# Optimization experiments

Hardware: AMD Instinct MI355X
Metric: run time of the kernel (lower is better)

The kernel has to match this reference:

```python
import jax, jax.numpy as jnp
import numpy as np


def setup_inputs() -> dict:
    key = jax.random.key(0)
    ks = jax.random.split(key, 15)
    B, r, d, h, na = 64, 64, 2048, 64, 256
    x = jax.random.normal(ks[0], (B, d, na), dtype=jnp.float32)
    L = jax.random.randint(ks[1], (B, 2, na), 0, 2).astype(jnp.float32)
    p = lambda i, shp: jax.random.normal(ks[i], shp, dtype=jnp.float32)
    return {
        "x": x, "L": L,
        "Aq": p(2, (r, d)), "Ak": p(3, (r, d)), "Av": p(4, (r, d)),
        "Aq1": p(5, (r, r)), "Ak1": p(6, (r, r)), "Av1": p(7, (r, r)),
        "Aq5": p(8, (r, r)), "Ak5": p(9, (r, r)), "Av5": p(10, (r, r)),
        "Ao": p(11, (r, r)), "Ao1": p(12, (r, r)), "Ao5": p(13, (h, r)),
    }


def reference(x, L, Aq, Ak, Av, Aq1, Ak1, Av1, Aq5, Ak5, Av5, Ao, Ao1, Ao5):
    B, d, na = x.shape
    # numNeighbors: count of L[:,0,:] >= 1 per batch, +1 -> [B,1,1]
    numN = jnp.sum((L[:, 0, :] >= 1.0).astype(jnp.float32), axis=1)[:, None, None] + 1.0
    scale = jnp.sqrt(numN)  # [B,1,1]

    def attn(M, Wq, Wk, Wv):
        # M: [B, f, na]; Wq/Wk/Wv: [r, f]
        Q = jax.nn.sigmoid(jnp.einsum('rf,bfn->bnr', Wq, M))  # [B,na,r]
        K = jax.nn.sigmoid(jnp.einsum('rf,bfn->brn', Wk, M))  # [B,r,na]
        V = jax.nn.sigmoid(jnp.einsum('rf,bfn->bnr', Wv, M))  # [B,na,r]
        A = jax.nn.softmax(jnp.einsum('bnr,brm->bnm', Q, K) / scale, axis=2)
        return jnp.einsum('bnm,bmr->brn', A, V)  # [B,r,na]

    o = attn(x, Aq, Ak, Av)
    M = jax.nn.silu(jnp.einsum('sr,brn->bsn', Ao, o))
    o = attn(M, Aq1, Ak1, Av1)
    M = jax.nn.silu(jnp.einsum('sr,brn->bsn', Ao1, o))
    o = attn(M, Aq5, Ak5, Av5)
    M = jax.nn.silu(jnp.einsum('hr,brn->bhn', Ao5, o))  # [B,h,na]

    blk = d // na  # rows per block (8)
    def diagvec(i):
        # kron(sum-of-squares, ones(1,2)) == repeat each element twice -> [B, 2*na]
        return jnp.repeat(jnp.sum(M[:, i * blk:(i + 1) * blk, :] ** 2, axis=1), 2, axis=1)

    M11, M12, M21, M22 = diagvec(0), diagvec(1), diagvec(2), diagvec(3)
    Mpp = jnp.sum(M[:, 4 * blk:, :] ** 2, axis=1)  # [B, na]

    # q = x[:, :4, :].transpose(1,2).reshape(B, 4*na) (agent-major ordering)
    q = jnp.transpose(x[:, :4, :], (0, 2, 1)).reshape(B, 4 * na)
    q1, q2 = q[:, :2 * na], q[:, 2 * na:]
    # Block matrix [[diag(M11), diag(M12)], [diag(M21), diag(M22)]] quadratic form,
    # computed without materializing the [B, 4na, 4na] matrix.
    quad = jnp.sum(M11 * q1 * q1 + M12 * q1 * q2 + M21 * q2 * q1 + M22 * q2 * q2,
                   axis=1, keepdims=True)
    return quad + jnp.sum(Mpp, axis=1, keepdims=True)  # [B, 1]
```

## Files before the change

kernel.cpp:

```cpp
#include <hip/hip_runtime.h>
#include <stdint.h>

typedef _Float16 f16;
typedef f16 f16x8 __attribute__((ext_vector_type(8)));
typedef float f32x4 __attribute__((ext_vector_type(4)));

#define MFMA(a,b,c) __builtin_amdgcn_mfma_f32_16x16x32_f16(a, b, c, 0, 0, 0)

__device__ __forceinline__ float sigmoidf_(float z) {
  return __builtin_amdgcn_rcpf(1.0f + __expf(-z));
}

__global__ void prep_kernel(const float* __restrict__ L,
    const float* __restrict__ Aq, const float* __restrict__ Ak, const float* __restrict__ Av,
    const float* __restrict__ Aq1, const float* __restrict__ Ak1, const float* __restrict__ Av1,
    const float* __restrict__ Aq5, const float* __restrict__ Ak5, const float* __restrict__ Av5,
    const float* __restrict__ Ao, const float* __restrict__ Ao1, const float* __restrict__ Ao5,
    float* __restrict__ scale, f16* __restrict__ Wcat, f16* __restrict__ Wsm,
    float* __restrict__ out)
{
  __shared__ float r4[4];
  int blk = blockIdx.x, t = threadIdx.x;
  if (blk < 64) {
    float v = (L[blk * 512 + t] >= 1.0f) ? 1.0f : 0.0f;
    #pragma unroll
    for (int off = 32; off; off >>= 1) v += __shfl_down(v, off);
    if ((t & 63) == 0) r4[t >> 6] = v;
    __syncthreads();
    if (t == 0) scale[blk] = sqrtf(r4[0] + r4[1] + r4[2] + r4[3] + 1.0f);
  } else if (blk < 160) {
    int base = (blk - 64) * 4096;
    for (int i = 0; i < 16; i++) {
      int idx = base + t + i * 256;
      int row = idx >> 11, col = idx & 2047;
      float v = (row < 64) ? Aq[row * 2048 + col]
              : (row < 128) ? Ak[(row - 64) * 2048 + col]
              : Av[(row - 128) * 2048 + col];
      Wcat[idx] = (f16)v;
    }
  } else if (blk < 169) {
    int j = blk - 160;
    const float* s = (j == 0) ? Aq1 : (j == 1) ? Ak1 : (j == 2) ? Av1 : (j == 3) ? Aq5
                   : (j == 4) ? Ak5 : (j == 5) ? Av5 : (j == 6) ? Ao : (j == 7) ? Ao1 : Ao5;
    for (int i = 0; i < 16; i++) { int idx = t + i * 256; Wsm[j * 4096 + idx] = (f16)s[idx]; }
  } else {
    if (t < 64) out[t] = 0.0f;
  }
}

__global__ __launch_bounds__(512, 4) void qkv1_kernel(const float* __restrict__ x,
    const f16* __restrict__ Wcat, f16* __restrict__ Qt, f16* __restrict__ Kt,
    f16* __restrict__ Vg)
{
  int b = blockIdx.y, n0 = blockIdx.x * 64;
  int t = threadIdx.x, lane = t & 63, w = t >> 6;
  int l15 = lane & 15, q = lane >> 4;
  __shared__ f16 xt[2][64 * 72];
  __shared__ f16 wt[2][192 * 72];
  f32x4 acc[2][3] = {};
  const float* xb = x + (size_t)b * 524288 + n0;
  int tn = t & 63, fg = t >> 6;
  int nh = w >> 2, wr_ = w & 3;

  int r0 = t >> 3,           c0 = t & 7;
  int r1 = (t + 512) >> 3,   c1 = (t + 512) & 7;
  int r2 = (t + 1024) >> 3,  c2 = (t + 1024) & 7;
  const f16* pw0 = Wcat + (size_t)r0 * 2048 + c0 * 8;
  const f16* pw1 = Wcat + (size_t)r1 * 2048 + c1 * 8;
  const f16* pw2 = Wcat + (size_t)r2 * 2048 + c2 * 8;
  const float* px = xb + (size_t)(fg * 8) * 256 + tn;

  float xa0, xa1, xa2, xa3, xa4, xa5, xa6, xa7;
  uint4 wr0, wr1, wr2;

#define LOAD_X(f0n) do {                                                        \
    const float* xp_ = px + (size_t)(f0n) * 256;                                \
    xa0 = xp_[0];    xa1 = xp_[256];  xa2 = xp_[512];  xa3 = xp_[768];          \
    xa4 = xp_[1024]; xa5 = xp_[1280]; xa6 = xp_[1536]; xa7 = xp_[1792];         \
  } while (0)

#define LOAD_W(f0n) do {                                                        \
    wr0 = *(const uint4*)(pw0 + (f0n)); wr1 = *(const uint4*)(pw1 + (f0n));     \
    wr2 = *(const uint4*)(pw2 + (f0n));                                         \
  } while (0)

#define WRITE_XW(buf) do {                                                      \
    f16x8 pk_;                                                                  \
    pk_[0] = (f16)xa0; pk_[1] = (f16)xa1; pk_[2] = (f16)xa2; pk_[3] = (f16)xa3; \
    pk_[4] = (f16)xa4; pk_[5] = (f16)xa5; pk_[6] = (f16)xa6; pk_[7] = (f16)xa7; \
    *(f16x8*)&xt[buf][tn * 72 + fg * 8] = pk_;                                  \
    f16* wb_ = &wt[buf][0];                                                     \
    *(uint4*)&wb_[r0 * 72 + c0 * 8] = wr0;                                      \
    *(uint4*)&wb_[r1 * 72 + c1 * 8] = wr1;                                      \
    *(uint4*)&wb_[r2 * 72 + c2 * 8] = wr2;                                      \
  } while (0)

  LOAD_X(0);
  LOAD_W(0);
  WRITE_XW(0);
  __syncthreads();

  int cur = 0;
  for (int f0 = 0; f0 < 2048; f0 += 64) {
    int nxt = cur ^ 1;
    bool more = (f0 + 64 < 2048);
    if (more) { LOAD_X(f0 + 64); LOAD_W(f0 + 64); }

    #pragma unroll
    for (int ks = 0; ks < 2; ks++) {
      int k0 = ks * 32 + q * 8;
      f16x8 af[2], bf[3];
      af[0] = *(const f16x8*)&xt[cur][(nh * 32 + l15) * 72 + k0];
      af[1] = *(const f16x8*)&xt[cur][(nh * 32 + 16 + l15) * 72 + k0];
      #pragma unroll
      for (int j = 0; j < 3; j++)
        bf[j] = *(const f16x8*)&wt[cur][((wr_ * 3 + j) * 16 + l15) * 72 + k0];
      #pragma unroll
      for (int nt = 0; nt < 2; nt++)
        #pragma unroll
        for (int j = 0; j < 3; j++)
          acc[nt][j] = MFMA(af[nt], bf[j], acc[nt][j]);
    }

    if (more) WRITE_XW(nxt);
    __syncthreads();
    cur = nxt;
  }
#undef LOAD_X
#undef LOAD_W
#undef WRITE_XW

  #pragma unroll
  for (int nt = 0; nt < 2; nt++)
    #pragma unroll
    for (int j = 0; j < 3; j++) {
      int rr = (wr_ * 3 + j) * 16 + l15;
      float s[4];
      #pragma unroll
      for (int reg = 0; reg < 4; reg++) s[reg] = sigmoidf_(acc[nt][j][reg]);
      int nbase = n0 + nh * 32 + nt * 16 + q * 4;
      if (rr < 64) {
        #pragma unroll
        for (int reg = 0; reg < 4; reg++)
          Qt[(size_t)b * 16384 + (size_t)(nbase + reg) * 64 + rr] = (f16)s[reg];
      } else if (rr < 128) {
        #pragma unroll
        for (int reg = 0; reg < 4; reg++)
          Kt[(size_t)b * 16384 + (size_t)(nbase + reg) * 64 + (rr - 64)] = (f16)s[reg];
      } else {
        union { f16 h[4]; uint2 u; } pk;
        #pragma unroll
        for (int reg = 0; reg < 4; reg++) pk.h[reg] = (f16)s[reg];
        *(uint2*)(Vg + (size_t)b * 16384 + (size_t)(rr - 128) * 256 + nbase) = pk.u;
      }
    }
}

template<int LAYER>
__global__ __launch_bounds__(1024) void attnB_kernel(const float* __restrict__ x,
    const float* __restrict__ scale, const f16* __restrict__ Wsm,
    const f16* __restrict__ Qtg, const f16* __restrict__ Ktg, const f16* __restrict__ Vgg,
    const f16* __restrict__ Min, f16* __restrict__ Mout, float* __restrict__ out)
{
  int g = blockIdx.x, b = blockIdx.y, n0 = g * 64;
  int t = threadIdx.x, lane = t & 63, w = t >> 6;
  int l15 = lane & 15, q = lane >> 4;
  __shared__ f16 KT[256 * 72];
  __shared__ f16 SM[256 * 72];
  __shared__ f16 VM[64 * 264];
  __shared__ f16 QT[64 * 72];
  __shared__ f16 OT[64 * 72];
  __shared__ float denomS[64];

  float sinv = __builtin_amdgcn_rcpf(scale[b]);
  if (t < 64) denomS[t] = 0.0f;

  if (LAYER == 0) {
    if (t < 512) {
      const uint4* qs = (const uint4*)(Qtg + (size_t)b * 16384 + (size_t)n0 * 64);
      int n = t >> 3, c = t & 7; *(uint4*)&QT[n * 72 + c * 8] = qs[t];
    }
    const uint4* ks = (const uint4*)(Ktg + (size_t)b * 16384);
    const uint4* vs = (const uint4*)(Vgg + (size_t)b * 16384);
    #pragma unroll
    for (int i = 0; i < 2; i++) {
      int id = t + i * 1024;
      int m = id >> 3, c = id & 7;
      *(uint4*)&KT[m * 72 + c * 8] = ks[id];
      int r = id >> 5, c2 = id & 31;
      *(uint4*)&VM[r * 264 + c2 * 8] = vs[id];
    }
  } else {
    const uint4* ms = (const uint4*)(Min + (size_t)b * 16384);
    #pragma unroll
    for (int i = 0; i < 2; i++) {
      int id = t + i * 1024, m = id >> 3, c = id & 7;
      *(uint4*)&SM[m * 72 + c * 8] = ms[id];
    }
  }
  __syncthreads();

  const f16* Wq = Wsm + (size_t)(LAYER == 1 ? 0 : 3) * 4096;
  const f16* Wk = Wsm + (size_t)(LAYER == 1 ? 1 : 4) * 4096;
  const f16* Wv = Wsm + (size_t)(LAYER == 1 ? 2 : 5) * 4096;
  const f16* Wo = Wsm + (size_t)(LAYER == 0 ? 6 : (LAYER == 1 ? 7 : 8)) * 4096;

  if (LAYER > 0) {
    if (w < 8) {
      f16x8 bk[4][2];
      #pragma unroll
      for (int rt = 0; rt < 4; rt++) {
        bk[rt][0] = *(const f16x8*)(Wk + (rt * 16 + l15) * 64 + q * 8);
        bk[rt][1] = *(const f16x8*)(Wk + (rt * 16 + l15) * 64 + 32 + q * 8);
      }
      #pragma unroll
      for (int mi = 0; mi < 2; mi++) {
        int mt = w * 2 + mi;
        f16x8 a0 = *(const f16x8*)&SM[(mt * 16 + l15) * 72 + q * 8];
        f16x8 a1 = *(const f16x8*)&SM[(mt * 16 + l15) * 72 + 32 + q * 8];
        #pragma unroll
        for (int rt = 0; rt < 4; rt++) {
          f32x4 acc = {}; acc = MFMA(a0, bk[rt][0], acc); acc = MFMA(a1, bk[rt][1], acc);
          #pragma unroll
          for (int reg = 0; reg < 4; reg++)
            KT[(mt * 16 + q * 4 + reg) * 72 + rt * 16 + l15] = (f16)sigmoidf_(acc[reg]);
        }
      }
    } else {
      f16x8 av[4][2];
      #pragma unroll
      for (int rt = 0; rt < 4; rt++) {
        av[rt][0] = *(const f16x8*)(Wv + (rt * 16 + l15) * 64 + q * 8);
        av[rt][1] = *(const f16x8*)(Wv + (rt * 16 + l15) * 64 + 32 + q * 8);
      }
      #pragma unroll
      for (int mi = 0; mi < 2; mi++) {
        int mt = (w - 8) * 2 + mi;
        f16x8 b0 = *(const f16x8*)&SM[(mt * 16 + l15) * 72 + q * 8];
        f16x8 b1 = *(const f16x8*)&SM[(mt * 16 + l15) * 72 + 32 + q * 8];
        #pragma unroll
        for (int rt = 0; rt < 4; rt++) {
          f32x4 acc = {}; acc = MFMA(av[rt][0], b0, acc); acc = MFMA(av[rt][1], b1, acc);
          #pragma unroll
          for (int reg = 0; reg < 4; reg++)
            VM[(rt * 16 + q * 4 + reg) * 264 + mt * 16 + l15] = (f16)sigmoidf_(acc[reg]);
        }
      }
    }
    {
      int nt = w >> 2, rt = w & 3;
      f16x8 a0 = *(const f16x8*)&SM[(n0 + nt * 16 + l15) * 72 + q * 8];
      f16x8 a1 = *(const f16x8*)&SM[(n0 + nt * 16 + l15) * 72 + 32 + q * 8];
      f16x8 b0 = *(const f16x8*)(Wq + (rt * 16 + l15) * 64 + q * 8);
      f16x8 b1 = *(const f16x8*)(Wq + (rt * 16 + l15) * 64 + 32 + q * 8);
      f32x4 acc = {}; acc = MFMA(a0, b0, acc); acc = MFMA(a1, b1, acc);
      #pragma unroll
      for (int reg = 0; reg < 4; reg++)
        QT[(nt * 16 + q * 4 + reg) * 72 + rt * 16 + l15] = (f16)sigmoidf_(acc[reg]);
    }
    __syncthreads();
  }

  {
    int nt = w >> 2;
    f16x8 a0 = *(const f16x8*)&QT[(nt * 16 + l15) * 72 + q * 8];
    f16x8 a1 = *(const f16x8*)&QT[(nt * 16 + l15) * 72 + 32 + q * 8];
    float dsum[4] = {0.f, 0.f, 0.f, 0.f};
    #pragma unroll
    for (int mi = 0; mi < 4; mi++) {
      int mt = (w & 3) * 4 + mi;
      f16x8 b0 = *(const f16x8*)&KT[(mt * 16 + l15) * 72 + q * 8];
      f16x8 b1 = *(const f16x8*)&KT[(mt * 16 + l15) * 72 + 32 + q * 8];
      f32x4 acc = {}; acc = MFMA(a0, b0, acc); acc = MFMA(a1, b1, acc);
      #pragma unroll
      for (int reg = 0; reg < 4; reg++) {
        float e = __expf(acc[reg] * sinv);
        dsum[reg] += e;
        SM[(nt * 16 + q * 4 + reg) * 264 + mt * 16 + l15] = (f16)e;
      }
    }
    #pragma unroll
    for (int reg = 0; reg < 4; reg++) {
      #pragma unroll
      for (int mask = 1; mask < 16; mask <<= 1) dsum[reg] += __shfl_xor(dsum[reg], mask);
    }
    if (l15 == 0) {
      #pragma unroll
      for (int reg = 0; reg < 4; reg++) atomicAdd(&denomS[nt * 16 + q * 4 + reg], dsum[reg]);
    }
  }
  __syncthreads();

  {
    int nt = w >> 2, rt = w & 3;
    f32x4 oacc = {};
    #pragma unroll
    for (int kc = 0; kc < 8; kc++) {
      f16x8 af = *(const f16x8*)&SM[(nt * 16 + l15) * 264 + kc * 32 + q * 8];
      f16x8 bf = *(const f16x8*)&VM[(rt * 16 + l15) * 264 + kc * 32 + q * 8];
      oacc = MFMA(af, bf, oacc);
    }
    float rden[4];
    #pragma unroll
    for (int reg = 0; reg < 4; reg++)
      rden[reg] = __builtin_amdgcn_rcpf(denomS[nt * 16 + q * 4 + reg]);
    #pragma unroll
    for (int reg = 0; reg < 4; reg++) {
      int row = nt * 16 + q * 4 + reg;
      OT[row * 72 + rt * 16 + l15] = (f16)(oacc[reg] * rden[reg]);
    }
  }
  __syncthreads();

  f16* Mst = QT;
  {
    int nt = w >> 2, st = w & 3;
    f16x8 a0 = *(const f16x8*)&OT[(nt * 16 + l15) * 72 + q * 8];
    f16x8 a1 = *(const f16x8*)&OT[(nt * 16 + l15) * 72 + 32 + q * 8];
    f16x8 b0 = *(const f16x8*)(Wo + (st * 16 + l15) * 64 + q * 8);
    f16x8 b1 = *(const f16x8*)(Wo + (st * 16 + l15) * 64 + 32 + q * 8);
    f32x4 acc = {}; acc = MFMA(a0, b0, acc); acc = MFMA(a1, b1, acc);
    #pragma unroll
    for (int reg = 0; reg < 4; reg++) {
      float z = acc[reg];
      Mst[(nt * 16 + q * 4 + reg) * 64 + st * 16 + l15] = (f16)(z * sigmoidf_(z));
    }
  }
  __syncthreads();

  if (LAYER < 2) {
    if (t < 512) {
      int row = t >> 3, c = t & 7;
      *(uint4*)(Mout + (size_t)b * 16384 + (size_t)(n0 + row) * 64 + c * 8)
          = *(const uint4*)&Mst[row * 64 + c * 8];
    }
  } else {
    float contrib = 0.0f;
    if (t < 64) {
      int ntok = n0 + t;
      const f16* row = &Mst[t * 64];
      float d[4] = {0, 0, 0, 0}, pp = 0.0f;
      #pragma unroll
      for (int gg = 0; gg < 8; gg++) {
        f16x8 v = *(const f16x8*)(row + gg * 8);
        float ss = 0.0f;
        #pragma unroll
        for (int k = 0; k < 8; k++) { float f = (float)v[k]; ss += f * f; }
        if (gg < 4) d[gg] = ss; else pp += ss;
      }
      int np = ntok >> 1, c0 = (ntok & 1) * 2;
      const float* xb = x + (size_t)b * 524288 + (size_t)c0 * 256;
      float q1a = xb[np], q1b = xb[256 + np];
      float q2a = xb[128 + np], q2b = xb[384 + np];
      contrib = d[0] * (q1a * q1a + q1b * q1b)
              + (d[1] + d[2]) * (q1a * q2a + q1b * q2b)
              + d[3] * (q2a * q2a + q2b * q2b) + pp;
    }
    if (w == 0) {
      #pragma unroll
      for (int off = 32; off; off >>= 1) contrib += __shfl_down(contrib, off);
      if (lane == 0) atomicAdd(out + b, contrib);
    }
  }
}

extern "C" void kernel_launch(void* const* d_in, const int* in_sizes, int n_in,
                              void* d_out, int out_size, void* d_ws, size_t ws_size,
                              hipStream_t stream) {
  const float* x   = (const float*)d_in[0];
  const float* L   = (const float*)d_in[1];
  const float* Aq  = (const float*)d_in[2];
  const float* Ak  = (const float*)d_in[3];
  const float* Av  = (const float*)d_in[4];
  const float* Aq1 = (const float*)d_in[5];
  const float* Ak1 = (const float*)d_in[6];
  const float* Av1 = (const float*)d_in[7];
  const float* Aq5 = (const float*)d_in[8];
  const float* Ak5 = (const float*)d_in[9];
  const float* Av5 = (const float*)d_in[10];
  const float* Ao  = (const float*)d_in[11];
  const float* Ao1 = (const float*)d_in[12];
  const float* Ao5 = (const float*)d_in[13];

  char* ws = (char*)d_ws;
  float* scale = (float*)ws;
  f16* Wcat  = (f16*)(ws + 256);
  f16* Wsm   = (f16*)(ws + 786688);
  f16* Qtg   = (f16*)(ws + 860416);
  f16* Ktg   = (f16*)(ws + 2957568);
  f16* Vgg   = (f16*)(ws + 5054720);
  f16* MbufA = (f16*)(ws + 7151872);
  f16* MbufB = (f16*)(ws + 9249024);
  float* out = (float*)d_out;

  prep_kernel<<<170, 256, 0, stream>>>(L, Aq, Ak, Av, Aq1, Ak1, Av1,
                                       Aq5, Ak5, Av5, Ao, Ao1, Ao5, scale, Wcat, Wsm, out);
  qkv1_kernel<<<dim3(4, 64), 512, 0, stream>>>(x, Wcat, Qtg, Ktg, Vgg);
  attnB_kernel<0><<<dim3(4, 64), 1024, 0, stream>>>(x, scale, Wsm, Qtg, Ktg, Vgg,
                                                    nullptr, MbufA, out);
  attnB_kernel<1><<<dim3(4, 64), 1024, 0, stream>>>(x, scale, Wsm, Qtg, Ktg, Vgg,
                                                    MbufA, MbufB, out);
  attnB_kernel<2><<<dim3(4, 64), 1024, 0, stream>>>(x, scale, Wsm, Qtg, Ktg, Vgg,
                                                    MbufB, nullptr, out);
}
```

Before: 265.6 us.

## Split QKV projection grid over output-row slices and smaller token tiles

The first QKV projection kernel moves from 256 blocks of 512 threads (64 tokens by all 192 output rows each) to 1536 blocks of 256 threads (32 tokens by one 64-row slice of Q, K or V). The aim is better occupancy and load balance across the GPU's compute units for this large-K GEMM, which previously had only 256 blocks. The cost is that each x tile is now loaded and converted to fp16 three times, once per row slice, and each weight tile is reused over fewer tokens, raising global memory traffic.

```diff
diff --git a/kernel.cpp b/kernel.cpp
--- a/kernel.cpp
+++ b/kernel.cpp
@@ -48,30 +48,28 @@
   }
 }
 
-__global__ __launch_bounds__(512, 4) void qkv1_kernel(const float* __restrict__ x,
+__global__ __launch_bounds__(256, 4) void qkv1_kernel(const float* __restrict__ x,
     const f16* __restrict__ Wcat, f16* __restrict__ Qt, f16* __restrict__ Kt,
     f16* __restrict__ Vg)
 {
-  int b = blockIdx.y, n0 = blockIdx.x * 64;
+  int rs = blockIdx.x, b = blockIdx.y, ng = blockIdx.z;
+  int n0 = ng * 32, rbase = rs * 64;
   int t = threadIdx.x, lane = t & 63, w = t >> 6;
   int l15 = lane & 15, q = lane >> 4;
-  __shared__ f16 xt[2][64 * 72];
-  __shared__ f16 wt[2][192 * 72];
-  f32x4 acc[2][3] = {};
+  __shared__ f16 xt[2][32 * 72];
+  __shared__ f16 wt[2][64 * 72];
+  f32x4 acc[2] = {};
   const float* xb = x + (size_t)b * 524288 + n0;
-  int tn = t & 63, fg = t >> 6;
-  int nh = w >> 2, wr_ = w & 3;
-
-  int r0 = t >> 3,           c0 = t & 7;
-  int r1 = (t + 512) >> 3,   c1 = (t + 512) & 7;
-  int r2 = (t + 1024) >> 3,  c2 = (t + 1024) & 7;
-  const f16* pw0 = Wcat + (size_t)r0 * 2048 + c0 * 8;
-  const f16* pw1 = Wcat + (size_t)r1 * 2048 + c1 * 8;
-  const f16* pw2 = Wcat + (size_t)r2 * 2048 + c2 * 8;
+  int tn = t & 31, fg = t >> 5;
+
+  int r0 = t >> 3,          c0 = t & 7;
+  int r1 = (t + 256) >> 3,  c1 = (t + 256) & 7;
+  const f16* pw0 = Wcat + (size_t)(rbase + r0) * 2048 + c0 * 8;
+  const f16* pw1 = Wcat + (size_t)(rbase + r1) * 2048 + c1 * 8;
   const float* px = xb + (size_t)(fg * 8) * 256 + tn;
 
   float xa0, xa1, xa2, xa3, xa4, xa5, xa6, xa7;
-  uint4 wr0, wr1, wr2;
+  uint4 wr0, wr1;
 
 #define LOAD_X(f0n) do {                                                        \
     const float* xp_ = px + (size_t)(f0n) * 256;                                \
@@ -81,7 +79,6 @@
 
 #define LOAD_W(f0n) do {                                                        \
     wr0 = *(const uint4*)(pw0 + (f0n)); wr1 = *(const uint4*)(pw1 + (f0n));     \
-    wr2 = *(const uint4*)(pw2 + (f0n));                                         \
   } while (0)
 
 #define WRITE_XW(buf) do {                                                      \
@@ -92,7 +89,6 @@
     f16* wb_ = &wt[buf][0];                                                     \
     *(uint4*)&wb_[r0 * 72 + c0 * 8] = wr0;                                      \
     *(uint4*)&wb_[r1 * 72 + c1 * 8] = wr1;                                      \
-    *(uint4*)&wb_[r2 * 72 + c2 * 8] = wr2;                                      \
   } while (0)
 
   LOAD_X(0);
@@ -109,17 +105,11 @@
     #pragma unroll
     for (int ks = 0; ks < 2; ks++) {
       int k0 = ks * 32 + q * 8;
-      f16x8 af[2], bf[3];
-      af[0] = *(const f16x8*)&xt[cur][(nh * 32 + l15) * 72 + k0];
-      af[1] = *(const f16x8*)&xt[cur][(nh * 32 + 16 + l15) * 72 + k0];
-      #pragma unroll
-      for (int j = 0; j < 3; j++)
-        bf[j] = *(const f16x8*)&wt[cur][((wr_ * 3 + j) * 16 + l15) * 72 + k0];
-      #pragma unroll
-      for (int nt = 0; nt < 2; nt++)
-        #pragma unroll
-        for (int j = 0; j < 3; j++)
-          acc[nt][j] = MFMA(af[nt], bf[j], acc[nt][j]);
+      f16x8 af0 = *(const f16x8*)&xt[cur][l15 * 72 + k0];
+      f16x8 af1 = *(const f16x8*)&xt[cur][(16 + l15) * 72 + k0];
+      f16x8 bf  = *(const f16x8*)&wt[cur][(w * 16 + l15) * 72 + k0];
+      acc[0] = MFMA(af0, bf, acc[0]);
+      acc[1] = MFMA(af1, bf, acc[1]);
     }
 
     if (more) WRITE_XW(nxt);
@@ -130,30 +120,28 @@
 #undef LOAD_W
 #undef WRITE_XW
 
+  int rr = rbase + w * 16 + l15;
   #pragma unroll
-  for (int nt = 0; nt < 2; nt++)
-    #pragma unroll
-    for (int j = 0; j < 3; j++) {
-      int rr = (wr_ * 3 + j) * 16 + l15;
-      float s[4];
-      #pragma unroll
-      for (int reg = 0; reg < 4; reg++) s[reg] = sigmoidf_(acc[nt][j][reg]);
-      int nbase = n0 + nh * 32 + nt * 16 + q * 4;
-      if (rr < 64) {
-        #pragma unroll
-        for (int reg = 0; reg < 4; reg++)
-          Qt[(size_t)b * 16384 + (size_t)(nbase + reg) * 64 + rr] = (f16)s[reg];
-      } else if (rr < 128) {
-        #pragma unroll
-        for (int reg = 0; reg < 4; reg++)
-          Kt[(size_t)b * 16384 + (size_t)(nbase + reg) * 64 + (rr - 64)] = (f16)s[reg];
-      } else {
-        union { f16 h[4]; uint2 u; } pk;
-        #pragma unroll
-        for (int reg = 0; reg < 4; reg++) pk.h[reg] = (f16)s[reg];
-        *(uint2*)(Vg + (size_t)b * 16384 + (size_t)(rr - 128) * 256 + nbase) = pk.u;
-      }
-    }
+  for (int nt = 0; nt < 2; nt++) {
+    float s[4];
+    #pragma unroll
+    for (int reg = 0; reg < 4; reg++) s[reg] = sigmoidf_(acc[nt][reg]);
+    int nbase = n0 + nt * 16 + q * 4;
+    if (rr < 64) {
+      #pragma unroll
+      for (int reg = 0; reg < 4; reg++)
+        Qt[(size_t)b * 16384 + (size_t)(nbase + reg) * 64 + rr] = (f16)s[reg];
+    } else if (rr < 128) {
+      #pragma unroll
+      for (int reg = 0; reg < 4; reg++)
+        Kt[(size_t)b * 16384 + (size_t)(nbase + reg) * 64 + (rr - 64)] = (f16)s[reg];
+    } else {
+      union { f16 h[4]; uint2 u; } pk;
+      #pragma unroll
+      for (int reg = 0; reg < 4; reg++) pk.h[reg] = (f16)s[reg];
+      *(uint2*)(Vg + (size_t)b * 16384 + (size_t)(rr - 128) * 256 + nbase) = pk.u;
+    }
+  }
 }
 
 template<int LAYER>
@@ -395,7 +383,7 @@
 
   prep_kernel<<<170, 256, 0, stream>>>(L, Aq, Ak, Av, Aq1, Ak1, Av1,
                                        Aq5, Ak5, Av5, Ao, Ao1, Ao5, scale, Wcat, Wsm, out);
-  qkv1_kernel<<<dim3(4, 64), 512, 0, stream>>>(x, Wcat, Qtg, Ktg, Vgg);
+  qkv1_kernel<<<dim3(3, 64, 8), 256, 0, stream>>>(x, Wcat, Qtg, Ktg, Vgg);
   attnB_kernel<0><<<dim3(4, 64), 1024, 0, stream>>>(x, scale, Wsm, Qtg, Ktg, Vgg,
                                                     nullptr, MbufA, out);
   attnB_kernel<1><<<dim3(4, 64), 1024, 0, stream>>>(x, scale, Wsm, Qtg, Ktg, Vgg,
```

Result: slower. 296.2 us (+11.5%).

## Retile qkv1 to 32-token blocks, pad LDS strides, hoist weight loads

Applied to the files above, without the earlier changes.

Halves the token tile in the QKV projection kernel to 32 with 256 threads and doubles the grid, so more blocks can run concurrently on the streaming x read. LDS row strides in both kernels are padded (72→76, 264→268, 64→68) to change bank mapping. In the attention kernel, weight fragments for K/V/Q projections are loaded from global before the staging barrier to overlap their latency. Risks: doubled weight reloads per token and 16-byte LDS accesses that are no longer 16-byte aligned.

```diff
diff --git a/kernel.cpp b/kernel.cpp
--- a/kernel.cpp
+++ b/kernel.cpp
@@ -48,30 +48,35 @@
   }
 }
 
-__global__ __launch_bounds__(512, 4) void qkv1_kernel(const float* __restrict__ x,
+__global__ __launch_bounds__(256) void qkv1_kernel(const float* __restrict__ x,
     const f16* __restrict__ Wcat, f16* __restrict__ Qt, f16* __restrict__ Kt,
     f16* __restrict__ Vg)
 {
-  int b = blockIdx.y, n0 = blockIdx.x * 64;
+  int b = blockIdx.y, n0 = blockIdx.x * 32;
   int t = threadIdx.x, lane = t & 63, w = t >> 6;
   int l15 = lane & 15, q = lane >> 4;
-  __shared__ f16 xt[2][64 * 72];
-  __shared__ f16 wt[2][192 * 72];
+  __shared__ f16 xt[2][32 * 76];
+  __shared__ f16 wt[2][192 * 76];
   f32x4 acc[2][3] = {};
   const float* xb = x + (size_t)b * 524288 + n0;
-  int tn = t & 63, fg = t >> 6;
-  int nh = w >> 2, wr_ = w & 3;
+  int tn = t & 31, fg = t >> 5;
 
   int r0 = t >> 3,           c0 = t & 7;
-  int r1 = (t + 512) >> 3,   c1 = (t + 512) & 7;
-  int r2 = (t + 1024) >> 3,  c2 = (t + 1024) & 7;
+  int r1 = (t + 256) >> 3,   c1 = (t + 256) & 7;
+  int r2 = (t + 512) >> 3,   c2 = (t + 512) & 7;
+  int r3 = (t + 768) >> 3,   c3 = (t + 768) & 7;
+  int r4 = (t + 1024) >> 3,  c4 = (t + 1024) & 7;
+  int r5 = (t + 1280) >> 3,  c5 = (t + 1280) & 7;
   const f16* pw0 = Wcat + (size_t)r0 * 2048 + c0 * 8;
   const f16* pw1 = Wcat + (size_t)r1 * 2048 + c1 * 8;
   const f16* pw2 = Wcat + (size_t)r2 * 2048 + c2 * 8;
+  const f16* pw3 = Wcat + (size_t)r3 * 2048 + c3 * 8;
+  const f16* pw4 = Wcat + (size_t)r4 * 2048 + c4 * 8;
+  const f16* pw5 = Wcat + (size_t)r5 * 2048 + c5 * 8;
   const float* px = xb + (size_t)(fg * 8) * 256 + tn;
 
   float xa0, xa1, xa2, xa3, xa4, xa5, xa6, xa7;
-  uint4 wr0, wr1, wr2;
+  uint4 wr0, wr1, wr2, wr3, wr4, wr5;
 
 #define LOAD_X(f0n) do {                                                        \
     const float* xp_ = px + (size_t)(f0n) * 256;                                \
@@ -81,18 +86,22 @@
 
 #define LOAD_W(f0n) do {                                                        \
     wr0 = *(const uint4*)(pw0 + (f0n)); wr1 = *(const uint4*)(pw1 + (f0n));     \
-    wr2 = *(const uint4*)(pw2 + (f0n));                                         \
+    wr2 = *(const uint4*)(pw2 + (f0n)); wr3 = *(const uint4*)(pw3 + (f0n));     \
+    wr4 = *(const uint4*)(pw4 + (f0n)); wr5 = *(const uint4*)(pw5 + (f0n));     \
   } while (0)
 
 #define WRITE_XW(buf) do {                                                      \
     f16x8 pk_;                                                                  \
     pk_[0] = (f16)xa0; pk_[1] = (f16)xa1; pk_[2] = (f16)xa2; pk_[3] = (f16)xa3; \
     pk_[4] = (f16)xa4; pk_[5] = (f16)xa5; pk_[6] = (f16)xa6; pk_[7] = (f16)xa7; \
-    *(f16x8*)&xt[buf][tn * 72 + fg * 8] = pk_;                                  \
+    *(f16x8*)&xt[buf][tn * 76 + fg * 8] = pk_;                                  \
     f16* wb_ = &wt[buf][0];                                                     \
-    *(uint4*)&wb_[r0 * 72 + c0 * 8] = wr0;                                      \
-    *(uint4*)&wb_[r1 * 72 + c1 * 8] = wr1;                                      \
-    *(uint4*)&wb_[r2 * 72 + c2 * 8] = wr2;                                      \
+    *(uint4*)&wb_[r0 * 76 + c0 * 8] = wr0;                                      \
+    *(uint4*)&wb_[r1 * 76 + c1 * 8] = wr1;                                      \
+    *(uint4*)&wb_[r2 * 76 + c2 * 8] = wr2;                                      \
+    *(uint4*)&wb_[r3 * 76 + c3 * 8] = wr3;                                      \
+    *(uint4*)&wb_[r4 * 76 + c4 * 8] = wr4;                                      \
+    *(uint4*)&wb_[r5 * 76 + c5 * 8] = wr5;                                      \
   } while (0)
 
   LOAD_X(0);
@@ -110,11 +119,10 @@
     for (int ks = 0; ks < 2; ks++) {
       int k0 = ks * 32 + q * 8;
       f16x8 af[2], bf[3];
-      af[0] = *(const f16x8*)&xt[cur][(nh * 32 + l15) * 72 + k0];
-      af[1] = *(const f16x8*)&xt[cur][(nh * 32 + 16 + l15) * 72 + k0];
-      #pragma unroll
-      for (int j = 0; j < 3; j++)
-        bf[j] = *(const f16x8*)&wt[cur][((wr_ * 3 + j) * 16 + l15) * 72 + k0];
+      af[0] = *(const f16x8*)&xt[cur][l15 * 76 + k0];
+      af[1] = *(const f16x8*)&xt[cur][(16 + l15) * 76 + k0];
+      #pragma unroll
+      for (int j = 0; j < 3; j++) bf[j] = *(const f16x8*)&wt[cur][((w * 3 + j) * 16 + l15) * 76 + k0];
       #pragma unroll
       for (int nt = 0; nt < 2; nt++)
         #pragma unroll
@@ -134,11 +142,11 @@
   for (int nt = 0; nt < 2; nt++)
     #pragma unroll
     for (int j = 0; j < 3; j++) {
-      int rr = (wr_ * 3 + j) * 16 + l15;
+      int rr = (w * 3 + j) * 16 + l15;
       float s[4];
       #pragma unroll
       for (int reg = 0; reg < 4; reg++) s[reg] = sigmoidf_(acc[nt][j][reg]);
-      int nbase = n0 + nh * 32 + nt * 16 + q * 4;
+      int nbase = n0 + nt * 16 + q * 4;
       if (rr < 64) {
         #pragma unroll
         for (int reg = 0; reg < 4; reg++)
@@ -165,118 +173,118 @@
   int g = blockIdx.x, b = blockIdx.y, n0 = g * 64;
   int t = threadIdx.x, lane = t & 63, w = t >> 6;
   int l15 = lane & 15, q = lane >> 4;
-  __shared__ f16 KT[256 * 72];
-  __shared__ f16 SM[256 * 72];
-  __shared__ f16 VM[64 * 264];
-  __shared__ f16 QT[64 * 72];
-  __shared__ f16 OT[64 * 72];
+  __shared__ f16 KT[256 * 76];
+  __shared__ f16 SM[256 * 76];
+  __shared__ f16 VM[64 * 268];
+  __shared__ f16 QT[64 * 76];
+  __shared__ f16 OT[64 * 76];
   __shared__ float denomS[64];
 
   float sinv = __builtin_amdgcn_rcpf(scale[b]);
   if (t < 64) denomS[t] = 0.0f;
-
-  if (LAYER == 0) {
-    if (t < 512) {
-      const uint4* qs = (const uint4*)(Qtg + (size_t)b * 16384 + (size_t)n0 * 64);
-      int n = t >> 3, c = t & 7; *(uint4*)&QT[n * 72 + c * 8] = qs[t];
-    }
-    const uint4* ks = (const uint4*)(Ktg + (size_t)b * 16384);
-    const uint4* vs = (const uint4*)(Vgg + (size_t)b * 16384);
-    #pragma unroll
-    for (int i = 0; i < 2; i++) {
-      int id = t + i * 1024;
-      int m = id >> 3, c = id & 7;
-      *(uint4*)&KT[m * 72 + c * 8] = ks[id];
-      int r = id >> 5, c2 = id & 31;
-      *(uint4*)&VM[r * 264 + c2 * 8] = vs[id];
-    }
-  } else {
-    const uint4* ms = (const uint4*)(Min + (size_t)b * 16384);
-    #pragma unroll
-    for (int i = 0; i < 2; i++) {
-      int id = t + i * 1024, m = id >> 3, c = id & 7;
-      *(uint4*)&SM[m * 72 + c * 8] = ms[id];
-    }
-  }
-  __syncthreads();
 
   const f16* Wq = Wsm + (size_t)(LAYER == 1 ? 0 : 3) * 4096;
   const f16* Wk = Wsm + (size_t)(LAYER == 1 ? 1 : 4) * 4096;
   const f16* Wv = Wsm + (size_t)(LAYER == 1 ? 2 : 5) * 4096;
   const f16* Wo = Wsm + (size_t)(LAYER == 0 ? 6 : (LAYER == 1 ? 7 : 8)) * 4096;
 
+  f16x8 bkav[4][2];
+  f16x8 wqa, wqb;
+  if (LAYER > 0) {
+    const f16* Wrole = (w < 8) ? Wk : Wv;
+    #pragma unroll
+    for (int rt = 0; rt < 4; rt++) {
+      bkav[rt][0] = *(const f16x8*)(Wrole + (rt * 16 + l15) * 64 + q * 8);
+      bkav[rt][1] = *(const f16x8*)(Wrole + (rt * 16 + l15) * 64 + 32 + q * 8);
+    }
+    int rtq = w & 3;
+    wqa = *(const f16x8*)(Wq + (rtq * 16 + l15) * 64 + q * 8);
+    wqb = *(const f16x8*)(Wq + (rtq * 16 + l15) * 64 + 32 + q * 8);
+  }
+
+  if (LAYER == 0) {
+    if (t < 512) {
+      const uint4* qs = (const uint4*)(Qtg + (size_t)b * 16384 + (size_t)n0 * 64);
+      int n = t >> 3, c = t & 7; *(uint4*)&QT[n * 76 + c * 8] = qs[t];
+    }
+    const uint4* ks = (const uint4*)(Ktg + (size_t)b * 16384);
+    const uint4* vs = (const uint4*)(Vgg + (size_t)b * 16384);
+    #pragma unroll
+    for (int i = 0; i < 2; i++) {
+      int id = t + i * 1024;
+      int m = id >> 3, c = id & 7;
+      *(uint4*)&KT[m * 76 + c * 8] = ks[id];
+      int r = id >> 5, c2 = id & 31;
+      *(uint4*)&VM[r * 268 + c2 * 8] = vs[id];
+    }
+  } else {
+    const uint4* ms = (const uint4*)(Min + (size_t)b * 16384);
+    #pragma unroll
+    for (int i = 0; i < 2; i++) {
+      int id = t + i * 1024, m = id >> 3, c = id & 7;
+      *(uint4*)&SM[m * 76 + c * 8] = ms[id];
+    }
+  }
+  __syncthreads();
+
   if (LAYER > 0) {
     if (w < 8) {
-      f16x8 bk[4][2];
-      #pragma unroll
-      for (int rt = 0; rt < 4; rt++) {
-        bk[rt][0] = *(const f16x8*)(Wk + (rt * 16 + l15) * 64 + q * 8);
-        bk[rt][1] = *(const f16x8*)(Wk + (rt * 16 + l15) * 64 + 32 + q * 8);
-      }
       #pragma unroll
       for (int mi = 0; mi < 2; mi++) {
         int mt = w * 2 + mi;
-        f16x8 a0 = *(const f16x8*)&SM[(mt * 16 + l15) * 72 + q * 8];
-        f16x8 a1 = *(const f16x8*)&SM[(mt * 16 + l15) * 72 + 32 + q * 8];
+        f16x8 a0 = *(const f16x8*)&SM[(mt * 16 + l15) * 76 + q * 8];
+        f16x8 a1 = *(const f16x8*)&SM[(mt * 16 + l15) * 76 + 32 + q * 8];
         #pragma unroll
         for (int rt = 0; rt < 4; rt++) {
-          f32x4 acc = {}; acc = MFMA(a0, bk[rt][0], acc); acc = MFMA(a1, bk[rt][1], acc);
+          f32x4 acc = {}; acc = MFMA(a0, bkav[rt][0], acc); acc = MFMA(a1, bkav[rt][1], acc);
           #pragma unroll
           for (int reg = 0; reg < 4; reg++)
-            KT[(mt * 16 + q * 4 + reg) * 72 + rt * 16 + l15] = (f16)sigmoidf_(acc[reg]);
+            KT[(mt * 16 + q * 4 + reg) * 76 + rt * 16 + l15] = (f16)sigmoidf_(acc[reg]);
         }
       }
     } else {
-      f16x8 av[4][2];
-      #pragma unroll
-      for (int rt = 0; rt < 4; rt++) {
-        av[rt][0] = *(const f16x8*)(Wv + (rt * 16 + l15) * 64 + q * 8);
-        av[rt][1] = *(const f16x8*)(Wv + (rt * 16 + l15) * 64 + 32 + q * 8);
-      }
       #pragma unroll
       for (int mi = 0; mi < 2; mi++) {
         int mt = (w - 8) * 2 + mi;
-        f16x8 b0 = *(const f16x8*)&SM[(mt * 16 + l15) * 72 + q * 8];
-        f16x8 b1 = *(const f16x8*)&SM[(mt * 16 + l15) * 72 + 32 + q * 8];
+        f16x8 b0 = *(const f16x8*)&SM[(mt * 16 + l15) * 76 + q * 8];
+        f16x8 b1 = *(const f16x8*)&SM[(mt * 16 + l15) * 76 + 32 + q * 8];
         #pragma unroll
         for (int rt = 0; rt < 4; rt++) {
-          f32x4 acc = {}; acc = MFMA(av[rt][0], b0, acc); acc = MFMA(av[rt][1], b1, acc);
+          f32x4 acc = {}; acc = MFMA(bkav[rt][0], b0, acc); acc = MFMA(bkav[rt][1], b1, acc);
           #pragma unroll
           for (int reg = 0; reg < 4; reg++)
-            VM[(rt * 16 + q * 4 + reg) * 264 + mt * 16 + l15] = (f16)sigmoidf_(acc[reg]);
+            VM[(rt * 16 + q * 4 + reg) * 268 + mt * 16 + l15] = (f16)sigmoidf_(acc[reg]);
         }
       }
     }
     {
       int nt = w >> 2, rt = w & 3;
-      f16x8 a0 = *(const f16x8*)&SM[(n0 + nt * 16 + l15) * 72 + q * 8];
-      f16x8 a1 = *(const f16x8*)&SM[(n0 + nt * 16 + l15) * 72 + 32 + q * 8];
-      f16x8 b0 = *(const f16x8*)(Wq + (rt * 16 + l15) * 64 + q * 8);
-      f16x8 b1 = *(const f16x8*)(Wq + (rt * 16 + l15) * 64 + 32 + q * 8);
-      f32x4 acc = {}; acc = MFMA(a0, b0, acc); acc = MFMA(a1, b1, acc);
+      f16x8 a0 = *(const f16x8*)&SM[(n0 + nt * 16 + l15) * 76 + q * 8];
+      f16x8 a1 = *(const f16x8*)&SM[(n0 + nt * 16 + l15) * 76 + 32 + q * 8];
+      f32x4 acc = {}; acc = MFMA(a0, wqa, acc); acc = MFMA(a1, wqb, acc);
       #pragma unroll
       for (int reg = 0; reg < 4; reg++)
-        QT[(nt * 16 + q * 4 + reg) * 72 + rt * 16 + l15] = (f16)sigmoidf_(acc[reg]);
+        QT[(nt * 16 + q * 4 + reg) * 76 + rt * 16 + l15] = (f16)sigmoidf_(acc[reg]);
     }
     __syncthreads();
   }
 
   {
     int nt = w >> 2;
-    f16x8 a0 = *(const f16x8*)&QT[(nt * 16 + l15) * 72 + q * 8];
-    f16x8 a1 = *(const f16x8*)&QT[(nt * 16 + l15) * 72 + 32 + q * 8];
+    f16x8 a0 = *(const f16x8*)&QT[(nt * 16 + l15) * 76 + q * 8];
+    f16x8 a1 = *(const f16x8*)&QT[(nt * 16 + l15) * 76 + 32 + q * 8];
     float dsum[4] = {0.f, 0.f, 0.f, 0.f};
     #pragma unroll
     for (int mi = 0; mi < 4; mi++) {
       int mt = (w & 3) * 4 + mi;
-      f16x8 b0 = *(const f16x8*)&KT[(mt * 16 + l15) * 72 + q * 8];
-      f16x8 b1 = *(const f16x8*)&KT[(mt * 16 + l15) * 72 + 32 + q * 8];
+      f16x8 b0 = *(const f16x8*)&KT[(mt * 16 + l15) * 76 + q * 8];
+      f16x8 b1 = *(const f16x8*)&KT[(mt * 16 + l15) * 76 + 32 + q * 8];
       f32x4 acc = {}; acc = MFMA(a0, b0, acc); acc = MFMA(a1, b1, acc);
       #pragma unroll
       for (int reg = 0; reg < 4; reg++) {
         float e = __expf(acc[reg] * sinv);
         dsum[reg] += e;
-        SM[(nt * 16 + q * 4 + reg) * 264 + mt * 16 + l15] = (f16)e;
+        SM[(nt * 16 + q * 4 + reg) * 268 + mt * 16 + l15] = (f16)e;
       }
     }
     #pragma unroll
@@ -296,8 +304,8 @@
     f32x4 oacc = {};
     #pragma unroll
     for (int kc = 0; kc < 8; kc++) {
-      f16x8 af = *(const f16x8*)&SM[(nt * 16 + l15) * 264 + kc * 32 + q * 8];
-      f16x8 bf = *(const f16x8*)&VM[(rt * 16 + l15) * 264 + kc * 32 + q * 8];
+      f16x8 af = *(const f16x8*)&SM[(nt * 16 + l15) * 268 + kc * 32 + q * 8];
+      f16x8 bf = *(const f16x8*)&VM[(rt * 16 + l15) * 268 + kc * 32 + q * 8];
       oacc = MFMA(af, bf, oacc);
     }
     float rden[4];
@@ -307,7 +315,7 @@
     #pragma unroll
     for (int reg = 0; reg < 4; reg++) {
       int row = nt * 16 + q * 4 + reg;
-      OT[row * 72 + rt * 16 + l15] = (f16)(oacc[reg] * rden[reg]);
+      OT[row * 76 + rt * 16 + l15] = (f16)(oacc[reg] * rden[reg]);
     }
   }
   __syncthreads();
@@ -315,15 +323,15 @@
   f16* Mst = QT;
   {
     int nt = w >> 2, st = w & 3;
-    f16x8 a0 = *(const f16x8*)&OT[(nt * 16 + l15) * 72 + q * 8];
-    f16x8 a1 = *(const f16x8*)&OT[(nt * 16 + l15) * 72 + 32 + q * 8];
+    f16x8 a0 = *(const f16x8*)&OT[(nt * 16 + l15) * 76 + q * 8];
+    f16x8 a1 = *(const f16x8*)&OT[(nt * 16 + l15) * 76 + 32 + q * 8];
     f16x8 b0 = *(const f16x8*)(Wo + (st * 16 + l15) * 64 + q * 8);
     f16x8 b1 = *(const f16x8*)(Wo + (st * 16 + l15) * 64 + 32 + q * 8);
     f32x4 acc = {}; acc = MFMA(a0, b0, acc); acc = MFMA(a1, b1, acc);
     #pragma unroll
     for (int reg = 0; reg < 4; reg++) {
       float z = acc[reg];
-      Mst[(nt * 16 + q * 4 + reg) * 64 + st * 16 + l15] = (f16)(z * sigmoidf_(z));
+      Mst[(nt * 16 + q * 4 + reg) * 68 + st * 16 + l15] = (f16)(z * sigmoidf_(z));
     }
   }
   __syncthreads();
@@ -332,13 +340,13 @@
     if (t < 512) {
       int row = t >> 3, c = t & 7;
       *(uint4*)(Mout + (size_t)b * 16384 + (size_t)(n0 + row) * 64 + c * 8)
-          = *(const uint4*)&Mst[row * 64 + c * 8];
+          = *(const uint4*)&Mst[row * 68 + c * 8];
     }
   } else {
     float contrib = 0.0f;
     if (t < 64) {
       int ntok = n0 + t;
-      const f16* row = &Mst[t * 64];
+      const f16* row = &Mst[t * 68];
       float d[4] = {0, 0, 0, 0}, pp = 0.0f;
       #pragma unroll
       for (int gg = 0; gg < 8; gg++) {
@@ -395,7 +403,7 @@
 
   prep_kernel<<<170, 256, 0, stream>>>(L, Aq, Ak, Av, Aq1, Ak1, Av1,
                                        Aq5, Ak5, Av5, Ao, Ao1, Ao5, scale, Wcat, Wsm, out);
-  qkv1_kernel<<<dim3(4, 64), 512, 0, stream>>>(x, Wcat, Qtg, Ktg, Vgg);
+  qkv1_kernel<<<dim3(8, 64), 256, 0, stream>>>(x, Wcat, Qtg, Ktg, Vgg);
   attnB_kernel<0><<<dim3(4, 64), 1024, 0, stream>>>(x, scale, Wsm, Qtg, Ktg, Vgg,
                                                     nullptr, MbufA, out);
   attnB_kernel<1><<<dim3(4, 64), 1024, 0, stream>>>(x, scale, Wsm, Qtg, Ktg, Vgg,
```

New measurement: 268.2 us. Within noise of the previous version (+1.0%).
